# Kernel optimization log

Measured on AMD Instinct MI355X. Metric: run time of the kernel, lower is better.

The kernel has to match this reference:

```python
import jax, jax.numpy as jnp
import numpy as np
from jax import lax

USER_NUM = 100000
COMP_NUM = 50000
ENTITY_NUM = USER_NUM + COMP_NUM + 2  # 150002
N_ACTIVE = USER_NUM + COMP_NUM        # 150000 valid graph nodes
REL_NUM = 200
D = 128
T = 12        # timesteps
E = 250000    # edges per timestep
S = 20000     # seed (LSTM-updated) nodes per timestep
B = 1024      # user batch
USER_ID_MAX = 99999


def setup_inputs() -> dict:
    key = jax.random.key(0)
    ks = jax.random.split(key, 16)
    ent_emb = jax.random.normal(ks[0], (ENTITY_NUM, D), jnp.float32) * 0.02
    c0_emb = jax.random.normal(ks[1], (ENTITY_NUM, D), jnp.float32) * 0.02
    rel_emb = jax.random.normal(ks[2], (REL_NUM, D), jnp.float32) * 0.02
    W_ih = jax.random.normal(ks[3], (4 * D, D), jnp.float32) * (1.0 / np.sqrt(D))
    W_hh = jax.random.normal(ks[4], (4 * D, D), jnp.float32) * (1.0 / np.sqrt(D))
    b_ih = jax.random.normal(ks[5], (4 * D,), jnp.float32) * 0.01
    b_hh = jax.random.normal(ks[6], (4 * D,), jnp.float32) * 0.01
    src = jax.random.randint(ks[7], (T, E), 0, N_ACTIVE, jnp.int32)
    dst = jax.random.randint(ks[8], (T, E), 0, N_ACTIVE, jnp.int32)
    rel_idx = jax.random.randint(ks[9], (T, E), 0, REL_NUM, jnp.int32)
    # unique seed nodes per timestep (scatter targets must not collide)
    seed_keys = jax.random.split(ks[10], T)
    seed_idx = jax.vmap(lambda k: jax.random.permutation(k, N_ACTIVE)[:S])(seed_keys).astype(jnp.int32)
    user_batch = jax.random.randint(ks[11], (B,), 0, USER_NUM, jnp.int32)
    comp_target = jax.random.randint(ks[12], (B,), 0, COMP_NUM, jnp.int32)
    job_target = jax.random.randint(ks[13], (B,), 0, REL_NUM // 2, jnp.int32)
    return {"ent_emb": ent_emb, "c0_emb": c0_emb, "rel_emb": rel_emb,
            "W_ih": W_ih, "W_hh": W_hh, "b_ih": b_ih, "b_hh": b_hh,
            "src": src, "dst": dst, "rel_idx": rel_idx, "seed_idx": seed_idx,
            "user_batch": user_batch, "comp_target": comp_target, "job_target": job_target}


def reference(ent_emb, c0_emb, rel_emb, W_ih, W_hh, b_ih, b_hh,
              src, dst, rel_idx, seed_idx, user_batch, comp_target, job_target):
    def step(carry, xs):
        h, c = carry                       # [N, D] node_emb / cx
        s, d, r, seed = xs
        # msg_GCN: m = src_node_emb * rel_emb[rel]; reduce_GCN: mean over mailbox
        m = h[s] * rel_emb[r]              # [E, D]
        msum = jax.ops.segment_sum(m, d, num_segments=ENTITY_NUM)
        cnt = jax.ops.segment_sum(jnp.ones((E,), h.dtype), d, num_segments=ENTITY_NUM)
        x = h + msum / jnp.maximum(cnt, 1.0)[:, None]   # update_node: node_emb + node_emb2
        # LSTMCell on seed nodes only (input = aggregated emb, state = pre-agg emb, cx)
        xi, hp, cp = x[seed], h[seed], c[seed]          # [S, D]
        gates = xi @ W_ih.T + b_ih + hp @ W_hh.T + b_hh  # [S, 4D]
        ig, fg, gg, og = jnp.split(gates, 4, axis=-1)
        cn = jax.nn.sigmoid(fg) * cp + jax.nn.sigmoid(ig) * jnp.tanh(gg)
        hn = jax.nn.sigmoid(og) * jnp.tanh(cn)
        return (x.at[seed].set(hn), c.at[seed].set(cn)), None

    (h, _c), _ = lax.scan(step, (ent_emb, c0_emb), (src, dst, rel_idx, seed_idx))

    u = h[user_batch]                                   # [B, D] user time embeddings
    # company softmax-CE (logsumexp over all companies)
    tc = ent_emb[comp_target + USER_ID_MAX + 1]
    all_c = ent_emb[USER_ID_MAX + 1: USER_ID_MAX + 1 + COMP_NUM]  # [COMP_NUM, D]
    pos_c = jnp.sum(u * tc, axis=1)
    comp_loss = -jnp.sum(pos_c - jax.nn.logsumexp(u @ all_c.T, axis=1))
    # job (relation) softmax-CE over rel_num // 2 jobs
    tj = rel_emb[job_target]
    all_j = rel_emb[: REL_NUM // 2]
    pos_j = jnp.sum(u * tj, axis=1)
    job_loss = -jnp.sum(pos_j - jax.nn.logsumexp(u @ all_j.T, axis=1))
    return jnp.stack([comp_loss, job_loss])
```

## Files before the change

kernel.cpp:

```cpp
#include <hip/hip_runtime.h>
#include <math.h>

typedef __attribute__((ext_vector_type(8))) short short8;
typedef __attribute__((ext_vector_type(8))) unsigned short u16x8;
typedef __attribute__((ext_vector_type(4))) float f32x4;
typedef __attribute__((ext_vector_type(2))) float f32x2;
typedef long i64;

#define USER_NUM_  100000
#define COMP_NUM_  50000
#define EN         150002
#define REL_NUM_   200
#define DD         128
#define TT         12
#define EE         250000
#define SS         20000
#define BB         1024
#define PPART      125
#define TILES_PP   25
#define NB         37
#define BSH        12
#define CHUNK      4096
#define NCH        62

__device__ inline unsigned short f2bf(float f) {
    unsigned u = __float_as_uint(f);
    unsigned r = (u + 0x7fffu + ((u >> 16) & 1u)) >> 16;
    return (unsigned short)r;
}

__device__ inline float bf2f(unsigned short u) {
    return __uint_as_float((unsigned)u << 16);
}

__device__ inline void fp8x8_to_f(uint2 u, float f[8]) {
    f32x2 a = __builtin_amdgcn_cvt_pk_f32_fp8((int)u.x, false);
    f32x2 b = __builtin_amdgcn_cvt_pk_f32_fp8((int)u.x, true);
    f32x2 c = __builtin_amdgcn_cvt_pk_f32_fp8((int)u.y, false);
    f32x2 d = __builtin_amdgcn_cvt_pk_f32_fp8((int)u.y, true);
    f[0] = a[0]; f[1] = a[1]; f[2] = b[0]; f[3] = b[1];
    f[4] = c[0]; f[5] = c[1]; f[6] = d[0]; f[7] = d[1];
}

__device__ inline unsigned fp8x4_pack(float f0, float f1, float f2, float f3) {
    int v = __builtin_amdgcn_cvt_pk_fp8_f32(f0, f1, 0, false);
    v = __builtin_amdgcn_cvt_pk_fp8_f32(f2, f3, v, true);
    return (unsigned)v;
}

__device__ inline unsigned char f_to_fp8(float f) {
    return (unsigned char)(__builtin_amdgcn_cvt_pk_fp8_f32(f, f, 0, false) & 0xff);
}

__device__ inline float fp8_to_f(unsigned char b) {
    return __builtin_amdgcn_cvt_f32_fp8((int)b, 0);
}

__device__ inline float sigmoidf_(float x) { return 1.f / (1.f + __expf(-x)); }

__device__ inline void lse_push(float v, float& m, float& s) {
    if (v <= m) { s += __expf(v - m); }
    else { s = s * __expf(m - v) + 1.f; m = v; }
}

__device__ inline void lse_merge(float& M, float& S, float M2, float S2) {
    float Mn = fmaxf(M, M2);
    S = S * __expf(M - Mn) + S2 * __expf(M2 - Mn);
    M = Mn;
}

__global__ __launch_bounds__(256) void packBF_k(const float* __restrict__ src, ushort4* __restrict__ dst, int n4) {
    int i = blockIdx.x * 256 + threadIdx.x;
    if (i >= n4) return;
    float4 v = ((const float4*)src)[i];
    ushort4 o;
    o.x = f2bf(v.x); o.y = f2bf(v.y); o.z = f2bf(v.z); o.w = f2bf(v.w);
    dst[i] = o;
}

__global__ __launch_bounds__(256) void packF8_k(const float* __restrict__ src, unsigned* __restrict__ dst, int n4) {
    int i = blockIdx.x * 256 + threadIdx.x;
    if (i >= n4) return;
    float4 v = ((const float4*)src)[i];
    dst[i] = fp8x4_pack(v.x, v.y, v.z, v.w);
}

__global__ __launch_bounds__(256) void zero_i32_k(int* __restrict__ p, int n) {
    int i = blockIdx.x * 256 + threadIdx.x;
    if (i < n) p[i] = 0;
}

__global__ __launch_bounds__(256) void prepW_k(const float* __restrict__ Wih, const float* __restrict__ Whh,
                                               const float* __restrict__ bih, const float* __restrict__ bhh,
                                               unsigned char* __restrict__ Wt8, float* __restrict__ bsum) {
    int n = blockIdx.x;
    int k = threadIdx.x;
    float v = (k < 128) ? Wih[n * 128 + k] : Whh[n * 128 + (k - 128)];
    Wt8[n * 256 + k] = f_to_fp8(v);
    if (k == 0) bsum[n] = bih[n] + bhh[n];
}

__global__ __launch_bounds__(256) void binA_k(const int* __restrict__ dst, int* __restrict__ bcnt,
                                              int t0) {
    int slot = blockIdx.y;
    int tid = threadIdx.x;
    int c0 = blockIdx.x * CHUNK;
    int w = tid >> 6;
    __shared__ int lcnt[4][NB];
    for (int i = tid; i < 4 * NB; i += 256) ((int*)lcnt)[i] = 0;
    __syncthreads();
#pragma unroll
    for (int i = 0; i < 16; ++i) {
        int e = c0 + i * 256 + tid;
        if (e < EE) {
            int d = __builtin_nontemporal_load(&dst[(size_t)(t0 + slot) * EE + e]);
            atomicAdd(&lcnt[w][d >> BSH], 1);
        }
    }
    __syncthreads();
    if (tid < NB)
        atomicAdd(&bcnt[slot * NB + tid], lcnt[0][tid] + lcnt[1][tid] + lcnt[2][tid] + lcnt[3][tid]);
}

__global__ __launch_bounds__(64) void binScan_k(const int* __restrict__ bcnt, int* __restrict__ bbase,
                                                int* __restrict__ bcur, int nt) {
    int slot = threadIdx.x;
    if (slot >= nt) return;
    int b = 0;
    for (int c = 0; c < NB; ++c) {
        bbase[slot * (NB + 1) + c] = b;
        bcur[slot * NB + c] = b;
        b += bcnt[slot * NB + c];
    }
    bbase[slot * (NB + 1) + NB] = b;
}

__global__ __launch_bounds__(256) void binB_k(const int* __restrict__ src, const int* __restrict__ dst,
                                              const int* __restrict__ rel, int* __restrict__ bcur,
                                              int2* __restrict__ bucketed, int t0) {
    int slot = blockIdx.y;
    int tid = threadIdx.x;
    int c0 = blockIdx.x * CHUNK;
    __shared__ int lcnt[NB], lbase[NB], gbase[NB], lcur[NB];
    __shared__ int2 stage[CHUNK];
    if (tid < NB) lcnt[tid] = 0;
    __syncthreads();

    int myb[16]; int2 myv[16];
#pragma unroll
    for (int i = 0; i < 16; ++i) {
        int e = c0 + i * 256 + tid;
        if (e < EE) {
            size_t gi = (size_t)(t0 + slot) * EE + e;
            int d = __builtin_nontemporal_load(&dst[gi]);
            int s = __builtin_nontemporal_load(&src[gi]);
            int r = __builtin_nontemporal_load(&rel[gi]);
            myb[i] = d >> BSH;
            myv[i] = make_int2(d, s | (r << 18));
            atomicAdd(&lcnt[myb[i]], 1);
        } else myb[i] = -1;
    }
    __syncthreads();
    if (tid == 0) {
        int b = 0;
        for (int c = 0; c < NB; ++c) { lbase[c] = b; b += lcnt[c]; }
    }
    __syncthreads();
    if (tid < NB) {
        gbase[tid] = (lcnt[tid] > 0) ? atomicAdd(&bcur[slot * NB + tid], lcnt[tid]) : 0;
        lcur[tid] = lbase[tid];
    }
    __syncthreads();
#pragma unroll
    for (int i = 0; i < 16; ++i) {
        if (myb[i] >= 0) {
            int p = atomicAdd(&lcur[myb[i]], 1);
            stage[p] = myv[i];
        }
    }
    __syncthreads();
    int w = tid >> 6, lane = tid & 63;
    int2* bout = bucketed + (size_t)slot * EE;
    for (int b = w; b < NB; b += 4) {
        int cnt = lcnt[b], lb = lbase[b], gb = gbase[b];
        for (int j = lane; j < cnt; j += 64)
            bout[gb + j] = stage[lb + j];
    }
}

__global__ __launch_bounds__(256) void histscat_k(const int2* __restrict__ bucketed,
                                                  const int* __restrict__ bbase,
                                                  int* __restrict__ startp, int* __restrict__ pairs) {
    int b = blockIdx.x, slot = blockIdx.y;
    int tid = threadIdx.x;
    int base_ent = b << BSH;
    int nloc = EN - base_ent; if (nloc > 4096) nloc = 4096;
    __shared__ int lcnt[4096];
    __shared__ int tsum[256];
    for (int i = tid; i < 4096; i += 256) lcnt[i] = 0;
    __syncthreads();
    int e0 = bbase[slot * (NB + 1) + b], e1 = bbase[slot * (NB + 1) + b + 1];
    const int2* bin = bucketed + (size_t)slot * EE;
    for (int e = e0 + tid; e < e1; e += 256)
        atomicAdd(&lcnt[bin[e].x - base_ent], 1);
    __syncthreads();
    int base16 = tid * 16;
    int s = 0;
#pragma unroll
    for (int k = 0; k < 16; ++k) s += lcnt[base16 + k];
    tsum[tid] = s;
    __syncthreads();
#pragma unroll
    for (int o = 1; o < 256; o <<= 1) {
        int x = (tid >= o) ? tsum[tid - o] : 0;
        __syncthreads();
        tsum[tid] += x;
        __syncthreads();
    }
    int run = e0 + tsum[tid] - s;
#pragma unroll
    for (int k = 0; k < 16; ++k) {
        int c = lcnt[base16 + k];
        lcnt[base16 + k] = run;
        run += c;
    }
    __syncthreads();
    int* pout = pairs + (size_t)slot * EE;
    for (int e = e0 + tid; e < e1; e += 256) {
        int2 ed = bin[e];
        int pos = atomicAdd(&lcnt[ed.x - base_ent], 1);
        pout[pos] = ed.y;
    }
    __syncthreads();
    for (int i = tid; i < nloc; i += 256)
        startp[(size_t)slot * EN + base_ent + i] = lcnt[i];
}

__global__ __launch_bounds__(256) void agg_k(const unsigned char* __restrict__ hold,
                                             unsigned char* __restrict__ hnew,
                                             const unsigned short* __restrict__ Rbf,
                                             const int* __restrict__ endp_all,
                                             const int* __restrict__ pairs, int slot) {
    int tid = threadIdx.x;
    int d = blockIdx.x * 16 + (tid >> 4);
    int l = tid & 15;
    if (d >= EN) return;
    const int* endp = endp_all + (size_t)slot * EN;
    int e0 = (d > 0) ? endp[d - 1] : 0;
    int e1 = endp[d];
    const int* pp = pairs + (size_t)slot * EE;
    float acc[8];
#pragma unroll
    for (int j = 0; j < 8; ++j) acc[j] = 0.f;
    int e = e0;
    for (; e + 2 <= e1; e += 2) {
        int pk0 = pp[e], pk1 = pp[e + 1];
        uint2 h0 = *(const uint2*)(hold + (size_t)(pk0 & 0x3FFFF) * DD + l * 8);
        u16x8 r0 = *(const u16x8*)(Rbf + (size_t)(pk0 >> 18) * DD + l * 8);
        uint2 h1 = *(const uint2*)(hold + (size_t)(pk1 & 0x3FFFF) * DD + l * 8);
        u16x8 r1 = *(const u16x8*)(Rbf + (size_t)(pk1 >> 18) * DD + l * 8);
        float hf0[8], hf1[8];
        fp8x8_to_f(h0, hf0);
        fp8x8_to_f(h1, hf1);
#pragma unroll
        for (int j = 0; j < 8; ++j)
            acc[j] = fmaf(hf1[j], bf2f(r1[j]), fmaf(hf0[j], bf2f(r0[j]), acc[j]));
    }
    if (e < e1) {
        int pk0 = pp[e];
        uint2 h0 = *(const uint2*)(hold + (size_t)(pk0 & 0x3FFFF) * DD + l * 8);
        u16x8 r0 = *(const u16x8*)(Rbf + (size_t)(pk0 >> 18) * DD + l * 8);
        float hf0[8];
        fp8x8_to_f(h0, hf0);
#pragma unroll
        for (int j = 0; j < 8; ++j)
            acc[j] = fmaf(hf0[j], bf2f(r0[j]), acc[j]);
    }
    uint2 hd = *(const uint2*)(hold + (size_t)d * DD + l * 8);
    float hdf[8];
    fp8x8_to_f(hd, hdf);
    int c = e1 - e0;
    float inv = (c > 0) ? 1.f / (float)c : 0.f;
    float o[8];
#pragma unroll
    for (int j = 0; j < 8; ++j) o[j] = fmaf(acc[j], inv, hdf[j]);
    uint2 ov;
    ov.x = fp8x4_pack(o[0], o[1], o[2], o[3]);
    ov.y = fp8x4_pack(o[4], o[5], o[6], o[7]);
    *(uint2*)(hnew + (size_t)d * DD + l * 8) = ov;
}

__global__ __launch_bounds__(256) void lstm_k(const unsigned char* __restrict__ hold,
                                              unsigned char* __restrict__ hnew,
                                              unsigned short* __restrict__ cbuf,
                                              const unsigned char* __restrict__ Wt8,
                                              const float* __restrict__ bsum, const int* __restrict__ seed) {
    int w = threadIdx.x >> 6;
    int lane = threadIdx.x & 63;
    int lrow = lane & 15, lhi = lane >> 4;
    int m0 = blockIdx.x * 16;
    int w32 = w * 32;

    int sd_row = seed[m0 + lrow];
    const unsigned char* pxi = hnew + (size_t)sd_row * DD;
    const unsigned char* php = hold + (size_t)sd_row * DD;

    f32x4 acc[4][2];
#pragma unroll
    for (int g = 0; g < 4; ++g)
#pragma unroll
        for (int s = 0; s < 2; ++s)
            acc[g][s] = (f32x4){0.f, 0.f, 0.f, 0.f};

#pragma unroll
    for (int kk = 0; kk < 8; ++kk) {
        int klane = kk * 32 + lhi * 8;
        const unsigned char* p = (klane < 128) ? (pxi + klane) : (php + (klane - 128));
        i64 af = *(const i64*)p;
#pragma unroll
        for (int g = 0; g < 4; ++g)
#pragma unroll
            for (int s = 0; s < 2; ++s) {
                int col = g * 128 + w32 + s * 16 + lrow;
                i64 bf = *(const i64*)(Wt8 + (size_t)col * 256 + klane);
                acc[g][s] = __builtin_amdgcn_mfma_f32_16x16x32_fp8_fp8(af, bf, acc[g][s], 0, 0, 0);
            }
    }

    __syncthreads();

#pragma unroll
    for (int r = 0; r < 4; ++r) {
        int m = m0 + lhi * 4 + r;
        int sd = seed[m];
#pragma unroll
        for (int s = 0; s < 2; ++s) {
            int d = w32 + s * 16 + lrow;
            float ig = acc[0][s][r] + bsum[d];
            float fg = acc[1][s][r] + bsum[128 + d];
            float gg = acc[2][s][r] + bsum[256 + d];
            float og = acc[3][s][r] + bsum[384 + d];
            float cp = bf2f(cbuf[(size_t)sd * DD + d]);
            float cn = sigmoidf_(fg) * cp + sigmoidf_(ig) * tanhf(gg);
            float hn = sigmoidf_(og) * tanhf(cn);
            cbuf[(size_t)sd * DD + d] = f2bf(cn);
            hnew[(size_t)sd * DD + d] = f_to_fp8(hn);
        }
    }
}

__global__ __launch_bounds__(256) void packU_k(const unsigned char* __restrict__ hfin, const int* __restrict__ ub,
                                               short* __restrict__ Ubf) {
    int i = blockIdx.x * 256 + threadIdx.x;
    if (i >= BB * DD) return;
    int u = i >> 7, k = i & 127;
    Ubf[i] = (short)f2bf(fp8_to_f(hfin[(size_t)ub[u] * DD + k]));
}

__global__ __launch_bounds__(256) void comp_mfma_k(const short* __restrict__ Ubf, const short* __restrict__ Cbf,
                                                   float* __restrict__ partm, float* __restrict__ parts) {
    int tid = threadIdx.x;
    int w = tid >> 6, lane = tid & 63;
    int lrow = lane & 15, lhi = lane >> 4;
    int ubase = blockIdx.x * 128 + w * 32;
    int p = blockIdx.y;

    __shared__ __align__(16) short ct[2][16][136];

    short8 a[2][4];
#pragma unroll
    for (int s2 = 0; s2 < 2; ++s2)
#pragma unroll
        for (int kc = 0; kc < 4; ++kc)
            a[s2][kc] = *(const short8*)(Ubf + (size_t)(ubase + s2 * 16 + lrow) * DD + kc * 32 + lhi * 8);

    float s[2][4];
#pragma unroll
    for (int s2 = 0; s2 < 2; ++s2)
#pragma unroll
        for (int r = 0; r < 4; ++r) s[s2][r] = 0.f;

    int c0 = p * TILES_PP * 16;
    int srow = tid >> 4, scol = (tid & 15) * 8;
    {
        short8 v = *(const short8*)(Cbf + (size_t)(c0 + srow) * DD + scol);
        *(short8*)&ct[0][srow][scol] = v;
    }

    for (int tile = 0; tile < TILES_PP; ++tile) {
        int cur = tile & 1;
        short8 pf;
        bool hn = (tile + 1 < TILES_PP);
        if (hn)
            pf = *(const short8*)(Cbf + (size_t)(c0 + (tile + 1) * 16 + srow) * DD + scol);
        __syncthreads();
        if (hn) *(short8*)&ct[cur ^ 1][srow][scol] = pf;

        f32x4 acc0 = {0.f, 0.f, 0.f, 0.f};
        f32x4 acc1 = {0.f, 0.f, 0.f, 0.f};
#pragma unroll
        for (int kc = 0; kc < 4; ++kc) {
            short8 b = *(const short8*)&ct[cur][lrow][kc * 32 + lhi * 8];
            acc0 = __builtin_amdgcn_mfma_f32_16x16x32_bf16(a[0][kc], b, acc0, 0, 0, 0);
            acc1 = __builtin_amdgcn_mfma_f32_16x16x32_bf16(a[1][kc], b, acc1, 0, 0, 0);
        }
#pragma unroll
        for (int r = 0; r < 4; ++r) {
            s[0][r] += __expf(acc0[r]);
            s[1][r] += __expf(acc1[r]);
        }
    }

#pragma unroll
    for (int s2 = 0; s2 < 2; ++s2)
#pragma unroll
        for (int r = 0; r < 4; ++r) {
            float S = s[s2][r];
#pragma unroll
            for (int o = 1; o < 16; o <<= 1)
                S += __shfl_xor(S, o, 64);
            if (lrow == 0) {
                int u = ubase + s2 * 16 + lhi * 4 + r;
                partm[(size_t)u * PPART + p] = 0.f;
                parts[(size_t)u * PPART + p] = S;
            }
        }
}

__global__ __launch_bounds__(256) void finish2_k(const unsigned char* __restrict__ hfin,
                                                 const float* __restrict__ ent,
                                                 const float* __restrict__ rel, const int* __restrict__ ub,
                                                 const int* __restrict__ ct, const int* __restrict__ jt,
                                                 const float* __restrict__ partm, const float* __restrict__ parts,
                                                 float* __restrict__ out) {
    __shared__ float s_u[4][128];
    int w = threadIdx.x >> 6, lane = threadIdx.x & 63;
    int u = blockIdx.x * 4 + w;

    const unsigned char* up = hfin + (size_t)ub[u] * DD;
    float u0 = fp8_to_f(up[lane]), u1 = fp8_to_f(up[lane + 64]);
    s_u[w][lane] = u0;
    s_u[w][lane + 64] = u1;

    const float* tcp = ent + (size_t)(USER_NUM_ + ct[u]) * DD;
    float pc = u0 * tcp[lane] + u1 * tcp[lane + 64];
    const float* tjp = rel + (size_t)jt[u] * DD;
    float pj = u0 * tjp[lane] + u1 * tjp[lane + 64];
#pragma unroll
    for (int o = 1; o < 64; o <<= 1) {
        pc += __shfl_xor(pc, o, 64);
        pj += __shfl_xor(pj, o, 64);
    }

    float M = partm[(size_t)u * PPART + lane];
    float S = parts[(size_t)u * PPART + lane];
    if (lane + 64 < PPART)
        lse_merge(M, S, partm[(size_t)u * PPART + lane + 64], parts[(size_t)u * PPART + lane + 64]);
#pragma unroll
    for (int o = 1; o < 64; o <<= 1) {
        float M2 = __shfl_xor(M, o, 64);
        float S2 = __shfl_xor(S, o, 64);
        lse_merge(M, S, M2, S2);
    }
    float lse_c = M + logf(S);

    int j1 = lane, j2 = lane + 64;
    bool v2 = j2 < (REL_NUM_ / 2);
    const float* r1 = rel + (size_t)j1 * DD;
    const float* r2 = rel + (size_t)(v2 ? j2 : 0) * DD;
    float d1 = 0.f, d2 = 0.f;
#pragma unroll 16
    for (int k = 0; k < DD; ++k) {
        float uk = s_u[w][k];
        d1 = fmaf(uk, r1[k], d1);
        d2 = fmaf(uk, r2[k], d2);
    }
    float Mj = d1, Sj = 1.f;
    if (v2) lse_push(d2, Mj, Sj);
#pragma unroll
    for (int o = 1; o < 64; o <<= 1) {
        float M2 = __shfl_xor(Mj, o, 64);
        float S2 = __shfl_xor(Sj, o, 64);
        lse_merge(Mj, Sj, M2, S2);
    }
    float lse_j = Mj + logf(Sj);

    if (lane == 0) {
        atomicAdd(&out[0], lse_c - pc);
        atomicAdd(&out[1], lse_j - pj);
    }
}

static inline size_t rup(size_t x) { return (x + 255) & ~(size_t)255; }

extern "C" void kernel_launch(void* const* d_in, const int* in_sizes, int n_in,
                              void* d_out, int out_size, void* d_ws, size_t ws_size,
                              hipStream_t stream) {
    const float* ent_emb = (const float*)d_in[0];
    const float* c0_emb  = (const float*)d_in[1];
    const float* rel_emb = (const float*)d_in[2];
    const float* W_ih    = (const float*)d_in[3];
    const float* W_hh    = (const float*)d_in[4];
    const float* b_ih    = (const float*)d_in[5];
    const float* b_hh    = (const float*)d_in[6];
    const int* src       = (const int*)d_in[7];
    const int* dst       = (const int*)d_in[8];
    const int* rel_idx   = (const int*)d_in[9];
    const int* seed_idx  = (const int*)d_in[10];
    const int* ubatch    = (const int*)d_in[11];
    const int* ctarg     = (const int*)d_in[12];
    const int* jtarg     = (const int*)d_in[13];
    float* out = (float*)d_out;

    const size_t HB8 = rup((size_t)EN * DD);
    const size_t HBH = rup((size_t)EN * DD * 2);

    char* base = (char*)d_ws;
    unsigned char* h0   = (unsigned char*)base;
    unsigned char* h1   = (unsigned char*)(base + HB8);
    unsigned short* cbuf = (unsigned short*)(base + 2 * HB8);

    int* startp; int* pairs; int2* bucketed; int* bcnt; int* bbase; int* bcur;
    unsigned char* Wt8; float* bsumv; unsigned short* Rbf;
    auto place = [&](int NT) -> size_t {
        size_t o = 2 * HB8 + HBH;
        startp   = (int*)(base + o);  o += rup((size_t)NT * EN * 4);
        pairs    = (int*)(base + o);  o += rup((size_t)NT * EE * 4);
        bucketed = (int2*)(base + o); o += rup((size_t)NT * EE * 8);
        bcnt     = (int*)(base + o);  o += rup((size_t)NT * NB * 4);
        bbase    = (int*)(base + o);  o += rup((size_t)NT * (NB + 1) * 4);
        bcur     = (int*)(base + o);  o += rup((size_t)NT * NB * 4);
        Wt8      = (unsigned char*)(base + o); o += rup(512 * 256);
        bsumv    = (float*)(base + o); o += rup(512 * 4);
        Rbf      = (unsigned short*)(base + o); o += rup((size_t)REL_NUM_ * DD * 2);
        return o;
    };

    const int cands[6] = {12, 6, 4, 3, 2, 1};
    int NT = 1;
    for (int i = 0; i < 6; ++i) {
        if (place(cands[i]) <= ws_size) { NT = cands[i]; break; }
    }
    place(NT);

    char* q = (char*)cbuf;
    short* Cbf = (short*)q;            q += rup((size_t)COMP_NUM_ * DD * 2);
    short* Ubf = (short*)q;            q += rup((size_t)BB * DD * 2);
    float* partm = (float*)q;          q += rup((size_t)BB * PPART * 4);
    float* parts = (float*)q;

    hipMemsetAsync(d_out, 0, 2 * sizeof(float), stream);

    const int n4 = EN * DD / 4;
    const int gcpy = (n4 + 255) / 256;

    prepW_k<<<512, 256, 0, stream>>>(W_ih, W_hh, b_ih, b_hh, Wt8, bsumv);
    packF8_k<<<gcpy, 256, 0, stream>>>(ent_emb, (unsigned*)h0, n4);
    packBF_k<<<gcpy, 256, 0, stream>>>(c0_emb, (ushort4*)cbuf, n4);
    packBF_k<<<(REL_NUM_ * DD / 4 + 255) / 256, 256, 0, stream>>>(rel_emb, (ushort4*)Rbf, REL_NUM_ * DD / 4);

    auto build = [&](int t0, int nt) {
        zero_i32_k<<<(nt * NB + 255) / 256, 256, 0, stream>>>(bcnt, nt * NB);
        binA_k<<<dim3(NCH, nt), 256, 0, stream>>>(dst, bcnt, t0);
        binScan_k<<<1, 64, 0, stream>>>(bcnt, bbase, bcur, nt);
        binB_k<<<dim3(NCH, nt), 256, 0, stream>>>(src, dst, rel_idx, bcur, bucketed, t0);
        histscat_k<<<dim3(NB, nt), 256, 0, stream>>>(bucketed, bbase, startp, pairs);
    };

    unsigned char* hold = h0;
    unsigned char* hnew = h1;
    const int gagg = (EN + 15) / 16;

    for (int b0 = 0; b0 < TT; b0 += NT) {
        int nb = (TT - b0 < NT) ? (TT - b0) : NT;
        build(b0, nb);
        for (int k = 0; k < nb; ++k) {
            int t = b0 + k;
            agg_k<<<gagg, 256, 0, stream>>>(hold, hnew, Rbf, startp, pairs, k);
            lstm_k<<<SS / 16, 256, 0, stream>>>(hold, hnew, cbuf, Wt8, bsumv, seed_idx + (size_t)t * SS);
            unsigned char* tmp = hold; hold = hnew; hnew = tmp;
        }
    }

    packBF_k<<<(COMP_NUM_ * DD / 4 + 255) / 256, 256, 0, stream>>>(ent_emb + (size_t)USER_NUM_ * DD,
                                                                   (ushort4*)Cbf, COMP_NUM_ * DD / 4);
    packU_k<<<(BB * DD + 255) / 256, 256, 0, stream>>>(hold, ubatch, Ubf);
    comp_mfma_k<<<dim3(BB / 128, PPART), 256, 0, stream>>>(Ubf, Cbf, partm, parts);
    finish2_k<<<BB / 4, 256, 0, stream>>>(hold, ent_emb, rel_emb, ubatch, ctarg, jtarg,
                                          partm, parts, out);
}
```

Before: 961.7 us.

## Stage seed LSTM inputs contiguously from aggregation and double rows per LSTM block

A seed-position map is built for each timestep, and the aggregation kernel writes each seed node's aggregated row and previous row into a dense xh buffer. The LSTM kernel then reads its A operands contiguously instead of gathering them at random from hold/hnew, and each block handles 32 rows so every weight fragment load feeds two MFMAs. The cost is an extra memset and scatter kernel per build, one more per-node index lookup in agg, and more accumulator registers in lstm. The __syncthreads in lstm is also removed.

```diff
diff --git a/kernel.cpp b/kernel.cpp
--- a/kernel.cpp
+++ b/kernel.cpp
@@ -100,6 +100,13 @@
     if (k == 0) bsum[n] = bih[n] + bhh[n];
 }
 
+__global__ __launch_bounds__(256) void spos_k(const int* __restrict__ seed, int* __restrict__ seedpos,
+                                              int t0) {
+    int slot = blockIdx.y;
+    int i = blockIdx.x * 256 + threadIdx.x;
+    if (i < SS) seedpos[(size_t)slot * EN + seed[(size_t)(t0 + slot) * SS + i]] = i;
+}
+
 __global__ __launch_bounds__(256) void binA_k(const int* __restrict__ dst, int* __restrict__ bcnt,
                                               int t0) {
     int slot = blockIdx.y;
@@ -240,7 +247,9 @@
                                              unsigned char* __restrict__ hnew,
                                              const unsigned short* __restrict__ Rbf,
                                              const int* __restrict__ endp_all,
-                                             const int* __restrict__ pairs, int slot) {
+                                             const int* __restrict__ pairs,
+                                             const int* __restrict__ seedpos_all,
+                                             unsigned char* __restrict__ xh, int slot) {
     int tid = threadIdx.x;
     int d = blockIdx.x * 16 + (tid >> 4);
     int l = tid & 15;
@@ -288,9 +297,15 @@
     ov.x = fp8x4_pack(o[0], o[1], o[2], o[3]);
     ov.y = fp8x4_pack(o[4], o[5], o[6], o[7]);
     *(uint2*)(hnew + (size_t)d * DD + l * 8) = ov;
-}
-
-__global__ __launch_bounds__(256) void lstm_k(const unsigned char* __restrict__ hold,
+
+    int sp = seedpos_all[(size_t)slot * EN + d];
+    if (sp >= 0) {
+        *(uint2*)(xh + (size_t)sp * 256 + l * 8) = ov;
+        *(uint2*)(xh + (size_t)sp * 256 + 128 + l * 8) = hd;
+    }
+}
+
+__global__ __launch_bounds__(256) void lstm_k(const unsigned char* __restrict__ xh,
                                               unsigned char* __restrict__ hnew,
                                               unsigned short* __restrict__ cbuf,
                                               const unsigned char* __restrict__ Wt8,
@@ -298,53 +313,53 @@
     int w = threadIdx.x >> 6;
     int lane = threadIdx.x & 63;
     int lrow = lane & 15, lhi = lane >> 4;
-    int m0 = blockIdx.x * 16;
+    int m0 = blockIdx.x * 32;
     int w32 = w * 32;
 
-    int sd_row = seed[m0 + lrow];
-    const unsigned char* pxi = hnew + (size_t)sd_row * DD;
-    const unsigned char* php = hold + (size_t)sd_row * DD;
-
-    f32x4 acc[4][2];
-#pragma unroll
-    for (int g = 0; g < 4; ++g)
-#pragma unroll
-        for (int s = 0; s < 2; ++s)
-            acc[g][s] = (f32x4){0.f, 0.f, 0.f, 0.f};
+    f32x4 acc[2][4][2];
+#pragma unroll
+    for (int mi = 0; mi < 2; ++mi)
+#pragma unroll
+        for (int g = 0; g < 4; ++g)
+#pragma unroll
+            for (int s = 0; s < 2; ++s)
+                acc[mi][g][s] = (f32x4){0.f, 0.f, 0.f, 0.f};
 
 #pragma unroll
     for (int kk = 0; kk < 8; ++kk) {
         int klane = kk * 32 + lhi * 8;
-        const unsigned char* p = (klane < 128) ? (pxi + klane) : (php + (klane - 128));
-        i64 af = *(const i64*)p;
+        i64 af0 = *(const i64*)(xh + (size_t)(m0 + lrow) * 256 + klane);
+        i64 af1 = *(const i64*)(xh + (size_t)(m0 + 16 + lrow) * 256 + klane);
 #pragma unroll
         for (int g = 0; g < 4; ++g)
 #pragma unroll
             for (int s = 0; s < 2; ++s) {
                 int col = g * 128 + w32 + s * 16 + lrow;
                 i64 bf = *(const i64*)(Wt8 + (size_t)col * 256 + klane);
-                acc[g][s] = __builtin_amdgcn_mfma_f32_16x16x32_fp8_fp8(af, bf, acc[g][s], 0, 0, 0);
+                acc[0][g][s] = __builtin_amdgcn_mfma_f32_16x16x32_fp8_fp8(af0, bf, acc[0][g][s], 0, 0, 0);
+                acc[1][g][s] = __builtin_amdgcn_mfma_f32_16x16x32_fp8_fp8(af1, bf, acc[1][g][s], 0, 0, 0);
             }
     }
 
-    __syncthreads();
-
-#pragma unroll
-    for (int r = 0; r < 4; ++r) {
-        int m = m0 + lhi * 4 + r;
-        int sd = seed[m];
-#pragma unroll
-        for (int s = 0; s < 2; ++s) {
-            int d = w32 + s * 16 + lrow;
-            float ig = acc[0][s][r] + bsum[d];
-            float fg = acc[1][s][r] + bsum[128 + d];
-            float gg = acc[2][s][r] + bsum[256 + d];
-            float og = acc[3][s][r] + bsum[384 + d];
-            float cp = bf2f(cbuf[(size_t)sd * DD + d]);
-            float cn = sigmoidf_(fg) * cp + sigmoidf_(ig) * tanhf(gg);
-            float hn = sigmoidf_(og) * tanhf(cn);
-            cbuf[(size_t)sd * DD + d] = f2bf(cn);
-            hnew[(size_t)sd * DD + d] = f_to_fp8(hn);
+#pragma unroll
+    for (int mi = 0; mi < 2; ++mi) {
+#pragma unroll
+        for (int r = 0; r < 4; ++r) {
+            int m = m0 + mi * 16 + lhi * 4 + r;
+            int sd = seed[m];
+#pragma unroll
+            for (int s = 0; s < 2; ++s) {
+                int d = w32 + s * 16 + lrow;
+                float ig = acc[mi][0][s][r] + bsum[d];
+                float fg = acc[mi][1][s][r] + bsum[128 + d];
+                float gg = acc[mi][2][s][r] + bsum[256 + d];
+                float og = acc[mi][3][s][r] + bsum[384 + d];
+                float cp = bf2f(cbuf[(size_t)sd * DD + d]);
+                float cn = sigmoidf_(fg) * cp + sigmoidf_(ig) * tanhf(gg);
+                float hn = sigmoidf_(og) * tanhf(cn);
+                cbuf[(size_t)sd * DD + d] = f2bf(cn);
+                hnew[(size_t)sd * DD + d] = f_to_fp8(hn);
+            }
         }
     }
 }
@@ -521,12 +536,15 @@
     unsigned short* cbuf = (unsigned short*)(base + 2 * HB8);
 
     int* startp; int* pairs; int2* bucketed; int* bcnt; int* bbase; int* bcur;
+    int* seedpos; unsigned char* xh;
     unsigned char* Wt8; float* bsumv; unsigned short* Rbf;
     auto place = [&](int NT) -> size_t {
         size_t o = 2 * HB8 + HBH;
         startp   = (int*)(base + o);  o += rup((size_t)NT * EN * 4);
         pairs    = (int*)(base + o);  o += rup((size_t)NT * EE * 4);
         bucketed = (int2*)(base + o); o += rup((size_t)NT * EE * 8);
+        seedpos  = (int*)(base + o);  o += rup((size_t)NT * EN * 4);
+        xh       = (unsigned char*)(base + o); o += rup((size_t)SS * 256);
         bcnt     = (int*)(base + o);  o += rup((size_t)NT * NB * 4);
         bbase    = (int*)(base + o);  o += rup((size_t)NT * (NB + 1) * 4);
         bcur     = (int*)(base + o);  o += rup((size_t)NT * NB * 4);
@@ -565,6 +583,8 @@
         binScan_k<<<1, 64, 0, stream>>>(bcnt, bbase, bcur, nt);
         binB_k<<<dim3(NCH, nt), 256, 0, stream>>>(src, dst, rel_idx, bcur, bucketed, t0);
         histscat_k<<<dim3(NB, nt), 256, 0, stream>>>(bucketed, bbase, startp, pairs);
+        hipMemsetAsync(seedpos, 0xFF, (size_t)nt * EN * 4, stream);
+        spos_k<<<dim3((SS + 255) / 256, nt), 256, 0, stream>>>(seed_idx, seedpos, t0);
     };
 
     unsigned char* hold = h0;
@@ -576,8 +596,8 @@
         build(b0, nb);
         for (int k = 0; k < nb; ++k) {
             int t = b0 + k;
-            agg_k<<<gagg, 256, 0, stream>>>(hold, hnew, Rbf, startp, pairs, k);
-            lstm_k<<<SS / 16, 256, 0, stream>>>(hold, hnew, cbuf, Wt8, bsumv, seed_idx + (size_t)t * SS);
+            agg_k<<<gagg, 256, 0, stream>>>(hold, hnew, Rbf, startp, pairs, seedpos, xh, k);
+            lstm_k<<<SS / 32, 256, 0, stream>>>(xh, hnew, cbuf, Wt8, bsumv, seed_idx + (size_t)t * SS);
             unsigned char* tmp = hold; hold = hnew; hnew = tmp;
         }
     }
```

New measurement: 864.2 us. 1.11x faster.
